# Kernel optimization log

Hardware: AMD Instinct MI355X
Metric: run time of the kernel (lower is better)

Reference implementation:

```python
import jax, jax.numpy as jnp
import numpy as np

N = 100000      # nodes
E = 1600000     # edges
F_IN = 64       # node_features
F_OUT = 32      # output_size


def _cheb2(H, row, col, w_norm, theta, bias):
    # ChebConv K=2, sym normalization, lambda_max=2 (GCLSTM default):
    # L_hat = L - I = -D^{-1/2} A D^{-1/2}, so T0 = H, T1 = -A_norm H
    agg = jax.ops.segment_sum(w_norm[:, None] * H[col], row, num_segments=N)  # [N, F_OUT]
    return H @ theta[0] - agg @ theta[1] + bias


def setup_inputs() -> dict:
    key = jax.random.key(0)
    ks = jax.random.split(key, 24)
    inp = {}
    inp["x"] = jax.random.normal(ks[0], (N, F_IN), jnp.float32)
    inp["edge_index"] = jax.random.randint(ks[1], (2, E), 0, N)
    inp["edge_weight"] = jax.random.uniform(ks[2], (E,), jnp.float32)
    inp["h"] = jax.random.normal(ks[3], (N, F_OUT), jnp.float32)
    inp["c"] = jax.random.normal(ks[4], (N, F_OUT), jnp.float32)
    s_in = float(1.0 / np.sqrt(F_IN))
    s_out = float(1.0 / np.sqrt(F_OUT))
    i = 5
    for g in "ifco":
        inp[f"W_{g}"] = jax.random.uniform(ks[i], (F_IN, F_OUT), jnp.float32, -s_in, s_in); i += 1
        inp[f"b_{g}"] = jax.random.uniform(ks[i], (1, F_OUT), jnp.float32, -s_in, s_in); i += 1
        inp[f"theta_{g}"] = jax.random.uniform(ks[i], (2, F_OUT, F_OUT), jnp.float32, -s_out, s_out); i += 1
        inp[f"cb_{g}"] = jax.random.uniform(ks[i], (F_OUT,), jnp.float32, -s_out, s_out); i += 1
    inp["W_lin"] = jax.random.uniform(ks[i], (F_OUT, 1), jnp.float32, -s_out, s_out); i += 1
    inp["b_lin"] = jax.random.uniform(ks[i], (1,), jnp.float32, -s_out, s_out)
    return inp


def reference(x, edge_index, edge_weight, h, c,
              W_i, b_i, theta_i, cb_i,
              W_f, b_f, theta_f, cb_f,
              W_c, b_c, theta_c, cb_c,
              W_o, b_o, theta_o, cb_o,
              W_lin, b_lin):
    row, col = edge_index[0], edge_index[1]
    # symmetric normalization of edge weights (get_laplacian 'sym')
    deg = jax.ops.segment_sum(edge_weight, row, num_segments=N)
    dis = jnp.where(deg > 0, jax.lax.rsqrt(jnp.where(deg > 0, deg, 1.0)), 0.0)
    w_norm = dis[row] * edge_weight * dis[col]  # [E]
    # GCLSTM gates: input x through dense W, hidden h through ChebConv
    I = jax.nn.sigmoid(x @ W_i + _cheb2(h, row, col, w_norm, theta_i, cb_i) + b_i)
    Fg = jax.nn.sigmoid(x @ W_f + _cheb2(h, row, col, w_norm, theta_f, cb_f) + b_f)
    T = jnp.tanh(x @ W_c + _cheb2(h, row, col, w_norm, theta_c, cb_c) + b_c)
    C = Fg * c + I * T
    O = jax.nn.sigmoid(x @ W_o + _cheb2(h, row, col, w_norm, theta_o, cb_o) + b_o)
    H = O * jnp.tanh(C)
    # wrapper head: relu then Linear(out, 1)
    return jax.nn.relu(H) @ W_lin + b_lin  # [N, 1]
```

## Files before the change

### kernel.cpp

```cpp
#include <hip/hip_runtime.h>
#include <math.h>

#define NN 100000
#define NE 1600000
#define EPB 2048
#define NEB 782
#define NBUK 391
#define CAP 8192

#define DEGSCALE 16777216.0f

typedef __attribute__((ext_vector_type(8))) short bf16x8;
typedef __attribute__((ext_vector_type(4))) float f32x4;

#define MFMA(A, B, C) __builtin_amdgcn_mfma_f32_16x16x32_bf16(A, B, C, 0, 0, 0)

__device__ __forceinline__ float sigm(float z) { return 1.0f / (1.0f + expf(-z)); }

__device__ __forceinline__ void split1(float v, unsigned short* hi, unsigned short* lo) {
  unsigned u = __float_as_uint(v);
  *hi = (unsigned short)(u >> 16);
  float hf = __uint_as_float(u & 0xFFFF0000u);
  float lf = v - hf;
  *lo = (unsigned short)(__float_as_uint(lf) >> 16);
}

__device__ __forceinline__ void split8(const float* f, bf16x8* hi, bf16x8* lo) {
#pragma unroll
  for (int j = 0; j < 8; ++j) {
    unsigned short h, l;
    split1(f[j], &h, &l);
    (*hi)[j] = (short)h;
    (*lo)[j] = (short)l;
  }
}

__device__ __forceinline__ bf16x8 as_bf16x8(uint4 q) {
  union { uint4 q; bf16x8 v; } u;
  u.q = q;
  return u.v;
}

__device__ __forceinline__ void load8(const float4* p, int idx4, float* f) {
  float4 a = p[idx4];
  float4 b = p[idx4 + 1];
  f[0] = a.x; f[1] = a.y; f[2] = a.z; f[3] = a.w;
  f[4] = b.x; f[5] = b.y; f[6] = b.z; f[7] = b.w;
}


__global__ __launch_bounds__(256) void k_p1(const int* __restrict__ row,
                                            int* __restrict__ counts) {
  __shared__ int hist[NBUK];
  for (int i = threadIdx.x; i < NBUK; i += 256) hist[i] = 0;
  __syncthreads();
  int e0 = blockIdx.x * EPB;
  int e1 = min(e0 + EPB, NE);
  for (int e = e0 + (int)threadIdx.x; e < e1; e += 256)
    atomicAdd(&hist[row[e] >> 8], 1);
  __syncthreads();
  for (int i = threadIdx.x; i < NBUK; i += 256)
    counts[blockIdx.x * NBUK + i] = hist[i];
}

__global__ __launch_bounds__(256) void k_s1(int* __restrict__ counts,
                                            int* __restrict__ total) {
  __shared__ int arr[NEB];
  int b = blockIdx.x;
  for (int k = threadIdx.x; k < NEB; k += 256) arr[k] = counts[k * NBUK + b];
  __syncthreads();
  if (threadIdx.x == 0) {
    int run = 0;
    for (int k = 0; k < NEB; ++k) { int t = arr[k]; arr[k] = run; run += t; }
    total[b] = run;
  }
  __syncthreads();
  for (int k = threadIdx.x; k < NEB; k += 256) counts[k * NBUK + b] = arr[k];
}

__global__ __launch_bounds__(512) void k_s2(const int* __restrict__ total,
                                            int* __restrict__ bases) {
  __shared__ int s[512];
  int t = threadIdx.x;
  int v = (t < NBUK) ? total[t] : 0;
  s[t] = v;
  __syncthreads();
  for (int o = 1; o < 512; o <<= 1) {
    int a = (t >= o) ? s[t - o] : 0;
    __syncthreads();
    s[t] += a;
    __syncthreads();
  }
  if (t < NBUK) bases[t] = s[t] - v;
  if (t == 0) bases[NBUK] = NE;
}

__global__ __launch_bounds__(256) void k_p2(const int* __restrict__ row,
                                            const int* __restrict__ col,
                                            const float* __restrict__ ew,
                                            const int* __restrict__ rel,
                                            const int* __restrict__ bases,
                                            int2* __restrict__ colw) {
  __shared__ int cursor[NBUK];
  for (int i = threadIdx.x; i < NBUK; i += 256)
    cursor[i] = bases[i] + rel[blockIdx.x * NBUK + i];
  __syncthreads();
  int e0 = blockIdx.x * EPB;
  int e1 = min(e0 + EPB, NE);
  for (int e = e0 + (int)threadIdx.x; e < e1; e += 256) {
    int r = row[e];
    int c = col[e];
    float w = ew[e];
    int slot = atomicAdd(&cursor[r >> 8], 1);
    colw[slot] = make_int2(c | ((r & 255) << 17), __float_as_int(w));
  }
}

__global__ __launch_bounds__(256) void k_bucket(const int* __restrict__ bases,
                                               int2* __restrict__ colw,
                                               int* __restrict__ rowptr,
                                               float* __restrict__ dis) {
  __shared__ int2 stage[CAP];
  __shared__ int cnt[256], degfx[256], s[256], cursor[256];
  int b = blockIdx.x;
  int base = bases[b];
  int M = bases[b + 1] - base;
  if (M > CAP) M = CAP;
  int t = threadIdx.x;
  cnt[t] = 0;
  degfx[t] = 0;
  __syncthreads();
  for (int i = t; i < M; i += 256) {
    int2 e = colw[base + i];
    stage[i] = e;
    int rl = (e.x >> 17) & 255;
    atomicAdd(&cnt[rl], 1);
    unsigned fx = (unsigned)(__int_as_float(e.y) * DEGSCALE + 0.5f);
    atomicAdd((unsigned*)&degfx[rl], fx);
  }
  __syncthreads();
  int v = cnt[t];
  s[t] = v;
  __syncthreads();
  for (int o = 1; o < 256; o <<= 1) {
    int a = (t >= o) ? s[t - o] : 0;
    __syncthreads();
    s[t] += a;
    __syncthreads();
  }
  int excl = s[t] - v;
  int node = b * 256 + t;
  if (node <= NN) rowptr[node] = base + excl;
  if (node < NN) {
    unsigned fx = (unsigned)degfx[t];
    dis[node] = fx ? rsqrtf((float)fx * (1.0f / DEGSCALE)) : 0.0f;
  }
  cursor[t] = excl;
  __syncthreads();
  for (int i = t; i < M; i += 256) {
    int2 e = stage[i];
    int rl = (e.x >> 17) & 255;
    int r = atomicAdd(&cursor[rl], 1);
    colw[base + r] = e;
  }
}

__global__ __launch_bounds__(256) void k_agg(const int* __restrict__ rowptr,
                                             const int2* __restrict__ colw,
                                             const float* __restrict__ dis,
                                             const float4* __restrict__ h4,
                                             float4* __restrict__ agg4) {
  int n = (blockIdx.x * 256 + threadIdx.x) >> 6;
  if (n >= NN) return;
  int lane = threadIdx.x & 63;
  int es = lane >> 3;
  int fg = lane & 7;
  int s0 = rowptr[n];
  int s1 = rowptr[n + 1];
  float4 acc = make_float4(0.f, 0.f, 0.f, 0.f);
  for (int j = s0 + es; j < s1; j += 8) {
    int2 cw = colw[j];
    int c = cw.x & 0x1FFFF;
    float w = __int_as_float(cw.y) * dis[c];
    float4 hv = h4[c * 8 + fg];
    acc.x = fmaf(w, hv.x, acc.x);
    acc.y = fmaf(w, hv.y, acc.y);
    acc.z = fmaf(w, hv.z, acc.z);
    acc.w = fmaf(w, hv.w, acc.w);
  }
#pragma unroll
  for (int o = 8; o < 64; o <<= 1) {
    acc.x += __shfl_xor(acc.x, o, 64);
    acc.y += __shfl_xor(acc.y, o, 64);
    acc.z += __shfl_xor(acc.z, o, 64);
    acc.w += __shfl_xor(acc.w, o, 64);
  }
  if (es == 0) {
    float dn = dis[n];
    acc.x *= dn; acc.y *= dn; acc.z *= dn; acc.w *= dn;
    agg4[n * 8 + fg] = acc;
  }
}

struct PrepParams {
  const float* W[4];
  const float* T0[4];
  const float* T1[4];
  const float* b[4];
  const float* cb[4];
  uint4* fh;
  uint4* fl;
  float* bias;
};

__global__ __launch_bounds__(256) void k_prep(PrepParams pp) {
  int idx = blockIdx.x * 256 + threadIdx.x;
  if (idx < 2048) {
    int T = idx >> 6;
    int lane = idx & 63;
    int ncol = ((T & 7) * 16) + (lane & 15);
    int g = ncol >> 5;
    int c = ncol & 31;
    int kq = (lane >> 4) * 8;
    const float* mat;
    int kbase;
    if (T < 16) { mat = pp.W[g]; kbase = (T >> 3) * 32 + kq; }
    else if (T < 24) { mat = pp.T0[g]; kbase = kq; }
    else { mat = pp.T1[g]; kbase = kq; }
    unsigned hw[4], lw[4];
#pragma unroll
    for (int jj = 0; jj < 4; ++jj) {
      unsigned short h0, l0, h1, l1;
      split1(mat[(kbase + 2 * jj) * 32 + c], &h0, &l0);
      split1(mat[(kbase + 2 * jj + 1) * 32 + c], &h1, &l1);
      hw[jj] = (unsigned)h0 | ((unsigned)h1 << 16);
      lw[jj] = (unsigned)l0 | ((unsigned)l1 << 16);
    }
    pp.fh[idx] = make_uint4(hw[0], hw[1], hw[2], hw[3]);
    pp.fl[idx] = make_uint4(lw[0], lw[1], lw[2], lw[3]);
  }
  if (blockIdx.x == 0 && threadIdx.x < 128) {
    int g = threadIdx.x >> 5;
    int c = threadIdx.x & 31;
    pp.bias[threadIdx.x] = pp.b[g][c] + pp.cb[g][c];
  }
}

struct GmmParams {
  const float4* x4;
  const float4* h4;
  const float4* agg4;
  const float* cst;
  const uint4* fh;
  const uint4* fl;
  const float* bias;
  const float* wlin;
  const float* blin;
  float* out;
};

__global__ __launch_bounds__(256) void k_gmm(GmmParams p) {
  const int lane = threadIdx.x & 63;
  const int wv = threadIdx.x >> 6;
  const int m0 = blockIdx.x * 64 + wv * 16;
  const int mr = lane & 15;
  const int quad = lane >> 4;
  int m = m0 + mr;
  if (m >= NN) m = NN - 1;

  bf16x8 xh[2], xl[2], hh, hl, gh, gl;
  float f[8];
#pragma unroll
  for (int kt = 0; kt < 2; ++kt) {
    load8(p.x4, (m * 64 + kt * 32 + quad * 8) >> 2, f);
    split8(f, &xh[kt], &xl[kt]);
  }
  load8(p.h4, (m * 32 + quad * 8) >> 2, f);
  split8(f, &hh, &hl);
  load8(p.agg4, (m * 32 + quad * 8) >> 2, f);
#pragma unroll
  for (int j = 0; j < 8; ++j) f[j] = -f[j];
  split8(f, &gh, &gl);

  float wl0 = p.wlin[mr];
  float wl1 = p.wlin[mr + 16];
  float bl = p.blin[0];

  f32x4 acc[8];
#pragma unroll 2
  for (int nt = 0; nt < 8; ++nt) {
    float bv = p.bias[nt * 16 + mr];
    f32x4 a;
    a[0] = bv; a[1] = bv; a[2] = bv; a[3] = bv;
    bf16x8 b0h = as_bf16x8(p.fh[nt * 64 + lane]);
    bf16x8 b0l = as_bf16x8(p.fl[nt * 64 + lane]);
    bf16x8 b1h = as_bf16x8(p.fh[(8 + nt) * 64 + lane]);
    bf16x8 b1l = as_bf16x8(p.fl[(8 + nt) * 64 + lane]);
    bf16x8 t0h = as_bf16x8(p.fh[(16 + nt) * 64 + lane]);
    bf16x8 t0l = as_bf16x8(p.fl[(16 + nt) * 64 + lane]);
    bf16x8 t1h = as_bf16x8(p.fh[(24 + nt) * 64 + lane]);
    bf16x8 t1l = as_bf16x8(p.fl[(24 + nt) * 64 + lane]);
    a = MFMA(xh[0], b0h, a); a = MFMA(xh[0], b0l, a); a = MFMA(xl[0], b0h, a);
    a = MFMA(xh[1], b1h, a); a = MFMA(xh[1], b1l, a); a = MFMA(xl[1], b1h, a);
    a = MFMA(hh, t0h, a);    a = MFMA(hh, t0l, a);    a = MFMA(hl, t0h, a);
    a = MFMA(gh, t1h, a);    a = MFMA(gh, t1l, a);    a = MFMA(gl, t1h, a);
    acc[nt] = a;
  }

#pragma unroll
  for (int r = 0; r < 4; ++r) {
    int node = m0 + quad * 4 + r;
    int nc = node < NN ? node : NN - 1;
    float c0 = p.cst[nc * 32 + mr];
    float c1 = p.cst[nc * 32 + 16 + mr];
    float I0 = sigm(acc[0][r]), I1 = sigm(acc[1][r]);
    float F0 = sigm(acc[2][r]), F1 = sigm(acc[3][r]);
    float T0 = tanhf(acc[4][r]), T1 = tanhf(acc[5][r]);
    float O0 = sigm(acc[6][r]), O1 = sigm(acc[7][r]);
    float C0 = fmaf(F0, c0, I0 * T0);
    float C1 = fmaf(F1, c1, I1 * T1);
    float H0 = O0 * tanhf(C0);
    float H1 = O1 * tanhf(C1);
    float part = fmaf(fmaxf(H0, 0.f), wl0, fmaxf(H1, 0.f) * wl1);
#pragma unroll
    for (int s = 1; s < 16; s <<= 1) part += __shfl_xor(part, s, 64);
    if (mr == 0 && node < NN) p.out[node] = part + bl;
  }
}

extern "C" void kernel_launch(void* const* d_in, const int* in_sizes, int n_in,
                              void* d_out, int out_size, void* d_ws, size_t ws_size,
                              hipStream_t stream) {
  const float* x = (const float*)d_in[0];
  const int* row = (const int*)d_in[1];
  const int* col = row + NE;
  const float* ew = (const float*)d_in[2];
  const float* h = (const float*)d_in[3];
  const float* c = (const float*)d_in[4];

  float* ws = (float*)d_ws;
  float* dis = ws;
  int* rowptr = (int*)(ws + 100000);
  int* counts = (int*)(ws + 200004);
  int* total = (int*)(ws + 505766);
  int* bases = (int*)(ws + 506160);
  uint4* fh = (uint4*)(ws + 506552);
  uint4* fl = (uint4*)(ws + 514744);
  float* biasws = ws + 522936;
  int2* colw = (int2*)(ws + 523064);
  float* agg = ws + 523064 + 2 * NE;

  k_p1<<<NEB, 256, 0, stream>>>(row, counts);
  k_s1<<<NBUK, 256, 0, stream>>>(counts, total);
  k_s2<<<1, 512, 0, stream>>>(total, bases);
  k_p2<<<NEB, 256, 0, stream>>>(row, col, ew, counts, bases, colw);
  k_bucket<<<NBUK, 256, 0, stream>>>(bases, colw, rowptr, dis);

  PrepParams pp;
  for (int g = 0; g < 4; ++g) {
    pp.W[g] = (const float*)d_in[5 + 4 * g];
    pp.b[g] = (const float*)d_in[6 + 4 * g];
    pp.T0[g] = (const float*)d_in[7 + 4 * g];
    pp.T1[g] = pp.T0[g] + 1024;
    pp.cb[g] = (const float*)d_in[8 + 4 * g];
  }
  pp.fh = fh;
  pp.fl = fl;
  pp.bias = biasws;
  k_prep<<<8, 256, 0, stream>>>(pp);

  k_agg<<<(NN + 3) / 4, 256, 0, stream>>>(rowptr, colw, dis, (const float4*)h,
                                          (float4*)agg);

  GmmParams gp;
  gp.x4 = (const float4*)x;
  gp.h4 = (const float4*)h;
  gp.agg4 = (const float4*)agg;
  gp.cst = c;
  gp.fh = fh;
  gp.fl = fl;
  gp.bias = biasws;
  gp.wlin = (const float*)d_in[21];
  gp.blin = (const float*)d_in[22];
  gp.out = (float*)d_out;
  k_gmm<<<(NN + 63) / 64, 256, 0, stream>>>(gp);
}
```

Before: 266.6 us.

## Enlarge edge partition chunks, parallel-scan bucket offsets, and rework aggregation lane mapping

Edge partition blocks now cover 8192 edges instead of 2048, so there are 196 blocks. The per-bucket prefix sum in k_s1 changes from a serial loop on one thread to a 256-wide parallel Hillis-Steele scan, and the workspace offsets shrink to match. The aggregation kernel now gives each lane one edge and half a feature row, loading four float4 values, instead of one float4 per lane over 8 edges. This means more edges are processed in parallel per node, at the cost of more shuffle reductions and more registers. The larger partition blocks may lower occupancy in k_p1 and k_p2.

```diff
diff --git a/kernel.cpp b/kernel.cpp
--- a/kernel.cpp
+++ b/kernel.cpp
@@ -3,8 +3,8 @@
 
 #define NN 100000
 #define NE 1600000
-#define EPB 2048
-#define NEB 782
+#define EPB 8192
+#define NEB 196
 #define NBUK 391
 #define CAP 8192
 
@@ -65,17 +65,20 @@
 
 __global__ __launch_bounds__(256) void k_s1(int* __restrict__ counts,
                                             int* __restrict__ total) {
-  __shared__ int arr[NEB];
+  __shared__ int s[256];
   int b = blockIdx.x;
-  for (int k = threadIdx.x; k < NEB; k += 256) arr[k] = counts[k * NBUK + b];
-  __syncthreads();
-  if (threadIdx.x == 0) {
-    int run = 0;
-    for (int k = 0; k < NEB; ++k) { int t = arr[k]; arr[k] = run; run += t; }
-    total[b] = run;
-  }
-  __syncthreads();
-  for (int k = threadIdx.x; k < NEB; k += 256) counts[k * NBUK + b] = arr[k];
+  int t = threadIdx.x;
+  int v = (t < NEB) ? counts[t * NBUK + b] : 0;
+  s[t] = v;
+  __syncthreads();
+  for (int o = 1; o < 256; o <<= 1) {
+    int a = (t >= o) ? s[t - o] : 0;
+    __syncthreads();
+    s[t] += a;
+    __syncthreads();
+  }
+  if (t < NEB) counts[t * NBUK + b] = s[t] - v;
+  if (t == 255) total[b] = s[255];
 }
 
 __global__ __launch_bounds__(512) void k_s2(const int* __restrict__ total,
@@ -173,32 +176,46 @@
   int n = (blockIdx.x * 256 + threadIdx.x) >> 6;
   if (n >= NN) return;
   int lane = threadIdx.x & 63;
-  int es = lane >> 3;
-  int fg = lane & 7;
+  int slot = lane >> 1;
+  int half = lane & 1;
   int s0 = rowptr[n];
   int s1 = rowptr[n + 1];
-  float4 acc = make_float4(0.f, 0.f, 0.f, 0.f);
-  for (int j = s0 + es; j < s1; j += 8) {
+  float4 acc0 = make_float4(0.f, 0.f, 0.f, 0.f);
+  float4 acc1 = acc0, acc2 = acc0, acc3 = acc0;
+  for (int j = s0 + slot; j < s1; j += 32) {
     int2 cw = colw[j];
     int c = cw.x & 0x1FFFF;
     float w = __int_as_float(cw.y) * dis[c];
-    float4 hv = h4[c * 8 + fg];
-    acc.x = fmaf(w, hv.x, acc.x);
-    acc.y = fmaf(w, hv.y, acc.y);
-    acc.z = fmaf(w, hv.z, acc.z);
-    acc.w = fmaf(w, hv.w, acc.w);
-  }
-#pragma unroll
-  for (int o = 8; o < 64; o <<= 1) {
-    acc.x += __shfl_xor(acc.x, o, 64);
-    acc.y += __shfl_xor(acc.y, o, 64);
-    acc.z += __shfl_xor(acc.z, o, 64);
-    acc.w += __shfl_xor(acc.w, o, 64);
-  }
-  if (es == 0) {
+    const float4* hp = h4 + c * 8 + half * 4;
+    float4 h0 = hp[0], h1 = hp[1], h2 = hp[2], h3 = hp[3];
+    acc0.x = fmaf(w, h0.x, acc0.x); acc0.y = fmaf(w, h0.y, acc0.y);
+    acc0.z = fmaf(w, h0.z, acc0.z); acc0.w = fmaf(w, h0.w, acc0.w);
+    acc1.x = fmaf(w, h1.x, acc1.x); acc1.y = fmaf(w, h1.y, acc1.y);
+    acc1.z = fmaf(w, h1.z, acc1.z); acc1.w = fmaf(w, h1.w, acc1.w);
+    acc2.x = fmaf(w, h2.x, acc2.x); acc2.y = fmaf(w, h2.y, acc2.y);
+    acc2.z = fmaf(w, h2.z, acc2.z); acc2.w = fmaf(w, h2.w, acc2.w);
+    acc3.x = fmaf(w, h3.x, acc3.x); acc3.y = fmaf(w, h3.y, acc3.y);
+    acc3.z = fmaf(w, h3.z, acc3.z); acc3.w = fmaf(w, h3.w, acc3.w);
+  }
+#pragma unroll
+  for (int o = 2; o < 64; o <<= 1) {
+    acc0.x += __shfl_xor(acc0.x, o, 64); acc0.y += __shfl_xor(acc0.y, o, 64);
+    acc0.z += __shfl_xor(acc0.z, o, 64); acc0.w += __shfl_xor(acc0.w, o, 64);
+    acc1.x += __shfl_xor(acc1.x, o, 64); acc1.y += __shfl_xor(acc1.y, o, 64);
+    acc1.z += __shfl_xor(acc1.z, o, 64); acc1.w += __shfl_xor(acc1.w, o, 64);
+    acc2.x += __shfl_xor(acc2.x, o, 64); acc2.y += __shfl_xor(acc2.y, o, 64);
+    acc2.z += __shfl_xor(acc2.z, o, 64); acc2.w += __shfl_xor(acc2.w, o, 64);
+    acc3.x += __shfl_xor(acc3.x, o, 64); acc3.y += __shfl_xor(acc3.y, o, 64);
+    acc3.z += __shfl_xor(acc3.z, o, 64); acc3.w += __shfl_xor(acc3.w, o, 64);
+  }
+  if (lane < 2) {
     float dn = dis[n];
-    acc.x *= dn; acc.y *= dn; acc.z *= dn; acc.w *= dn;
-    agg4[n * 8 + fg] = acc;
+    float4* ap = agg4 + n * 8 + half * 4;
+    acc0.x *= dn; acc0.y *= dn; acc0.z *= dn; acc0.w *= dn;
+    acc1.x *= dn; acc1.y *= dn; acc1.z *= dn; acc1.w *= dn;
+    acc2.x *= dn; acc2.y *= dn; acc2.z *= dn; acc2.w *= dn;
+    acc3.x *= dn; acc3.y *= dn; acc3.z *= dn; acc3.w *= dn;
+    ap[0] = acc0; ap[1] = acc1; ap[2] = acc2; ap[3] = acc3;
   }
 }
 
@@ -342,13 +359,13 @@
   float* dis = ws;
   int* rowptr = (int*)(ws + 100000);
   int* counts = (int*)(ws + 200004);
-  int* total = (int*)(ws + 505766);
-  int* bases = (int*)(ws + 506160);
-  uint4* fh = (uint4*)(ws + 506552);
-  uint4* fl = (uint4*)(ws + 514744);
-  float* biasws = ws + 522936;
-  int2* colw = (int2*)(ws + 523064);
-  float* agg = ws + 523064 + 2 * NE;
+  int* total = (int*)(ws + 276640);
+  int* bases = (int*)(ws + 277032);
+  uint4* fh = (uint4*)(ws + 277424);
+  uint4* fl = (uint4*)(ws + 285616);
+  float* biasws = ws + 293808;
+  int2* colw = (int2*)(ws + 293936);
+  float* agg = ws + 293936 + 2 * NE;
 
   k_p1<<<NEB, 256, 0, stream>>>(row, counts);
   k_s1<<<NBUK, 256, 0, stream>>>(counts, total);
```

Result: slower. 302.8 us (+13.6%).
